# Optimization experiments

Measured on AMD Instinct MI355X. Metric: run time of the kernel, lower is better.

## Reference

```python
import jax, jax.numpy as jnp
import numpy as np

N = 50000      # nodes (single node type 'tx')
E = 400000     # edges per edge type ('fwd' and 'rev')
F_IN = 128     # input feature dim
F = 128        # cfg.gnn.dim_inner
H = 8          # attention heads
D = F // H     # per-head dim
L = 2          # cfg.gnn.layers_mp
C = 2          # dim_out (fraud logits)


def setup_inputs() -> dict:
    key = jax.random.key(0)
    k = jax.random.split(key, 12)
    f32 = jnp.float32
    g = lambda kk, sh, fan: jax.random.normal(kk, sh, f32) / np.float32(np.sqrt(fan))
    return dict(
        x=jax.random.normal(k[0], (N, F_IN), f32),
        edge_index_fwd=jax.random.randint(k[1], (2, E), 0, N),
        edge_index_rev=jax.random.randint(k[2], (2, E), 0, N),
        in_w=g(k[3], (F_IN, F), F_IN),
        in_b=jnp.zeros((F,), f32),
        kqv_w=g(k[4], (L, F, 3 * F), F),
        kqv_b=jnp.zeros((L, 3 * F), f32),
        krel_w=g(k[5], (L, 2, H, D, D), D),
        vrel_w=g(k[6], (L, 2, H, D, D), D),
        p_rel=jnp.ones((L, 2, H), f32),
        out_w=g(k[7], (L, F, F), F),
        out_b=jnp.zeros((L, F), f32),
        skip=jnp.ones((L,), f32),
        head_w=g(k[8], (F, C), F),
        head_b=jnp.zeros((C,), f32),
    )


def reference(x, edge_index_fwd, edge_index_rev, in_w, in_b, kqv_w, kqv_b,
              krel_w, vrel_w, p_rel, out_w, out_b, skip, head_w, head_b):
    n = x.shape[0]
    ef, er = edge_index_fwd, edge_index_rev
    Ef, Er = ef.shape[1], er.shape[1]
    dst = jnp.concatenate([ef[1], er[1]])                 # [E_tot]
    scale = 1.0 / jnp.sqrt(jnp.asarray(D, x.dtype))

    h = x @ in_w + in_b                                   # in_proj['tx'], [N,F]
    for l in range(L):
        kqv = h @ kqv_w[l] + kqv_b[l]                     # [N,3F]
        k, q, v = jnp.split(kqv, 3, axis=1)
        k = k.reshape(n, H, D)
        q = q.reshape(n, H, D)
        v = v.reshape(n, H, D)
        # per-edge-type relation transforms (head-wise DxD, no bias)
        k_rel = jnp.einsum('nhd,ehdf->enhf', k, krel_w[l])  # [2,N,H,D]
        v_rel = jnp.einsum('nhd,ehdf->enhf', v, vrel_w[l])
        # gather src features per edge type, concatenate edge types
        k_j = jnp.concatenate([k_rel[0][ef[0]], k_rel[1][er[0]]], axis=0)  # [E_tot,H,D]
        v_j = jnp.concatenate([v_rel[0][ef[0]], v_rel[1][er[0]]], axis=0)
        p_e = jnp.concatenate([jnp.broadcast_to(p_rel[l, 0], (Ef, H)),
                               jnp.broadcast_to(p_rel[l, 1], (Er, H))], axis=0)
        q_i = q[dst]                                       # [E_tot,H,D]
        alpha = jnp.einsum('ehd,ehd->eh', q_i, k_j) * p_e * scale
        # segment softmax over all incoming edges of each dst node
        m = jax.ops.segment_max(alpha, dst, num_segments=n)
        ex = jnp.exp(alpha - m[dst])
        denom = jax.ops.segment_sum(ex, dst, num_segments=n)
        w = ex / (denom[dst] + 1e-16)                      # [E_tot,H]
        agg = jax.ops.segment_sum(w[:, :, None] * v_j, dst,
                                  num_segments=n).reshape(n, F)
        a = jax.nn.gelu(agg, approximate=False) @ out_w[l] + out_b[l]
        g = jax.nn.sigmoid(skip[l])
        h = jax.nn.relu(g * a + (1.0 - g) * h)             # skip + act(dropout=0)
    return h @ head_w + head_b                             # logits [N,C]
```

## Files before the change

### kernel.cpp

```cpp
#include <hip/hip_runtime.h>
#include <math.h>

typedef short short8 __attribute__((ext_vector_type(8)));
typedef float f32x4 __attribute__((ext_vector_type(4)));

__device__ __forceinline__ unsigned short f2bf(float f){
    unsigned u = __float_as_uint(f);
    unsigned r = u + 0x7fffu + ((u >> 16) & 1u);
    return (unsigned short)(r >> 16);
}
__device__ __forceinline__ float bf2f(unsigned short s){
    return __uint_as_float((unsigned)s << 16);
}

__global__ void k_count(const int* __restrict__ ef, const int* __restrict__ er,
                        int* __restrict__ deg, int Ef, int Er)
{
    int Etot = Ef + Er;
    for (int e = blockIdx.x*blockDim.x + threadIdx.x; e < Etot; e += gridDim.x*blockDim.x) {
        int dst = (e < Ef) ? ef[Ef + e] : er[Er + (e - Ef)];
        atomicAdd(&deg[dst], 1);
    }
}

__global__ void k_chunk_sums(const int* __restrict__ deg, int* __restrict__ csum, int n)
{
    __shared__ int s[256];
    int t = threadIdx.x, i = blockIdx.x*256 + t;
    s[t] = (i < n) ? deg[i] : 0;
    __syncthreads();
    for (int off = 128; off > 0; off >>= 1) {
        if (t < off) s[t] += s[t + off];
        __syncthreads();
    }
    if (t == 0) csum[blockIdx.x] = s[0];
}

__global__ void k_scan_chunks(int* __restrict__ csum, int nch)
{
    __shared__ int s[1024];
    int t = threadIdx.x;
    int v = (t < nch) ? csum[t] : 0;
    s[t] = v; __syncthreads();
    for (int off = 1; off < 1024; off <<= 1) {
        int u = (t >= off) ? s[t - off] : 0;
        __syncthreads();
        s[t] += u;
        __syncthreads();
    }
    if (t < nch) csum[t] = s[t] - v;
}

__global__ void k_rowstart(const int* __restrict__ deg, const int* __restrict__ csum,
                           int* __restrict__ row_start, int* __restrict__ cursor, int n)
{
    __shared__ int s[256];
    int t = threadIdx.x, i = blockIdx.x*256 + t;
    int d = (i < n) ? deg[i] : 0;
    s[t] = d; __syncthreads();
    for (int off = 1; off < 256; off <<= 1) {
        int u = (t >= off) ? s[t - off] : 0;
        __syncthreads();
        s[t] += u;
        __syncthreads();
    }
    if (i <= n) {
        int rs = csum[blockIdx.x] + s[t] - d;
        row_start[i] = rs;
        cursor[i] = rs;
    }
}

__global__ void k_fill(const int* __restrict__ ef, const int* __restrict__ er,
                       int* __restrict__ cursor, unsigned* __restrict__ srcs,
                       int Ef, int Er, int n_nodes)
{
    int Etot = Ef + Er;
    if (blockIdx.x == 0 && threadIdx.x < 8) srcs[Etot + threadIdx.x] = 0;
    for (int e = blockIdx.x*blockDim.x + threadIdx.x; e < Etot; e += gridDim.x*blockDim.x) {
        int src, dst, tt;
        if (e < Ef) { src = ef[e]; dst = ef[Ef + e]; tt = 0; }
        else { int e2 = e - Ef; src = er[e2]; dst = er[Er + e2]; tt = 1; }
        int pos = atomicAdd(&cursor[dst], 1);
        srcs[pos] = (unsigned)(tt*n_nodes + src)*32u;
    }
}

__global__ void k_setup(const float* __restrict__ kqv_w, const float* __restrict__ kqv_b,
                        const float* __restrict__ krel_w, const float* __restrict__ vrel_w,
                        const float* __restrict__ p_rel, const float* __restrict__ out_w,
                        const float* __restrict__ out_b, const float* __restrict__ in_w,
                        const float* __restrict__ x, const float* __restrict__ head_b,
                        unsigned short* __restrict__ WcT, float* __restrict__ biasc,
                        unsigned short* __restrict__ WoT, float* __restrict__ biaso,
                        unsigned short* __restrict__ WiT, unsigned short* __restrict__ x16,
                        int* __restrict__ deg, float* __restrict__ logits, int n_nodes)
{
    const int N0 = 2*129*640;
    const int N1 = N0 + 2*129*128;
    const int N2 = N1 + 128*128;
    const long long N3 = (long long)N2 + (long long)n_nodes*32;
    const long long N4 = N3 + n_nodes;
    const long long N5 = N4 + 2*n_nodes;

    for (long long idx = (long long)blockIdx.x*blockDim.x + threadIdx.x; idx < N5;
         idx += (long long)gridDim.x*blockDim.x) {
        if (idx < N0) {
            int i = (int)idx;
            int l = i / (129*640);
            int rem = i % (129*640);
            int r = rem / 640, c = rem % 640;
            float val;
            if (c < 128) {
                val = (r < 128) ? kqv_w[((size_t)l*128 + r)*384 + 128 + c]
                                : kqv_b[l*384 + 128 + c];
            } else {
                int c2 = c - 128;
                int tt = c2 >> 8;
                int cc = c2 & 255;
                int f = cc >> 1;
                int part = cc & 1;
                int hh = f >> 4, fd = f & 15;
                const float* rw = (part == 0 ? krel_w : vrel_w)
                                  + (((size_t)(l*2 + tt)*8 + hh)*16)*16 + fd;
                int base_col = (part == 0 ? 0 : 256) + hh*16;
                float s = 0.f;
                #pragma unroll
                for (int d = 0; d < 16; ++d) {
                    float a = (r < 128) ? kqv_w[((size_t)l*128 + r)*384 + base_col + d]
                                        : kqv_b[l*384 + base_col + d];
                    s += a * rw[d*16];
                }
                if (part == 0) s *= p_rel[(l*2 + tt)*8 + hh] * 0.25f * 1.4426950408889634f;
                val = s;
            }
            if (r < 128) WcT[((size_t)l*640 + c)*128 + r] = f2bf(val);
            else         biasc[l*640 + c] = val;
        } else if (idx < N1) {
            int i = (int)(idx - N0);
            int l = i / (129*128);
            int rem = i % (129*128);
            int r = rem / 128, c = rem % 128;
            if (r < 128) WoT[((size_t)l*128 + c)*128 + r] = f2bf(out_w[((size_t)l*128 + r)*128 + c]);
            else         biaso[l*128 + c] = out_b[l*128 + c];
        } else if (idx < N2) {
            int i = (int)(idx - N1);
            int r = i >> 7, c = i & 127;
            WiT[(size_t)c*128 + r] = f2bf(in_w[(size_t)r*128 + c]);
        } else if (idx < N3) {
            long long i = idx - N2;
            float4 v = *(const float4*)&x[i*4];
            uint2 w;
            w.x = (unsigned)f2bf(v.x) | ((unsigned)f2bf(v.y) << 16);
            w.y = (unsigned)f2bf(v.z) | ((unsigned)f2bf(v.w) << 16);
            *(uint2*)&x16[i*4] = w;
        } else if (idx < N4) {
            deg[idx - N3] = 0;
        } else {
            long long i = idx - N4;
            logits[i] = head_b[i & 1];
        }
    }
}

__global__ __launch_bounds__(256) void k_mfma(
    const unsigned short* __restrict__ A16, const unsigned short* __restrict__ WT,
    const float* __restrict__ biasc, unsigned short* __restrict__ q16,
    unsigned short* __restrict__ h16, unsigned* __restrict__ kv,
    const float* __restrict__ skip, const float* __restrict__ hw,
    float* __restrict__ logits, int l,
    int n_nodes, int R, int C, int mode)
{
    __shared__ uint4 As[64*16];
    __shared__ uint4 Ws[64*16];
    int b = blockIdx.x;
    int xcd = b & 7, jj = b >> 3;
    int r_t = (jj / C)*8 + xcd;
    int c_t = jj % C;
    if (r_t >= R) return;
    int n0 = r_t*64, c0 = c_t*64;
    int t = threadIdx.x;

    #pragma unroll
    for (int it = 0; it < 4; ++it) {
        int gi = t + it*256;
        int m = gi >> 4, g = gi & 15;
        uint4 a = *(const uint4*)&A16[((size_t)(n0 + m)*16 + g)*8];
        As[m*16 + (g ^ (m & 15))] = a;
    }
    #pragma unroll
    for (int it = 0; it < 4; ++it) {
        int gi = t + it*256;
        int cw = gi >> 4, g = gi & 15;
        uint4 wv = *(const uint4*)&WT[((size_t)(c0 + cw)*16 + g)*8];
        Ws[cw*16 + (g ^ (cw & 15))] = wv;
    }
    __syncthreads();

    int lane = t & 63, w = t >> 6;
    int lm = lane & 15, quad = lane >> 4;
    f32x4 acc[4];
    #pragma unroll
    for (int i = 0; i < 4; ++i) { acc[i][0]=0.f; acc[i][1]=0.f; acc[i][2]=0.f; acc[i][3]=0.f; }

    #pragma unroll
    for (int chunk = 0; chunk < 4; ++chunk) {
        int gq = chunk*4 + quad;
        short8 bfrag = *(const short8*)&Ws[(w*16 + lm)*16 + (gq ^ lm)];
        #pragma unroll
        for (int i = 0; i < 4; ++i) {
            short8 afrag = *(const short8*)&As[(i*16 + lm)*16 + (gq ^ lm)];
            acc[i] = __builtin_amdgcn_mfma_f32_16x16x32_bf16(afrag, bfrag, acc[i], 0, 0, 0);
        }
    }

    int c = c0 + w*16 + lm;
    float bc = biasc[c];
    bool even = (lane & 1) == 0;
    if (mode == 3) {
        float g = 1.f/(1.f + expf(-skip[l]));
        float hw0 = hw[c*2], hw1 = hw[c*2 + 1];
        #pragma unroll
        for (int i = 0; i < 4; ++i) {
            #pragma unroll
            for (int rr = 0; rr < 4; ++rr) {
                int m = n0 + i*16 + quad*4 + rr;
                float nv = 0.f;
                if (m < n_nodes) {
                    float hv = bf2f(h16[(size_t)m*128 + c]);
                    nv = fmaxf(g*(acc[i][rr] + bc) + (1.f - g)*hv, 0.f);
                }
                float p0 = nv*hw0, p1 = nv*hw1;
                p0 += __shfl_xor(p0, 1); p1 += __shfl_xor(p1, 1);
                p0 += __shfl_xor(p0, 2); p1 += __shfl_xor(p1, 2);
                p0 += __shfl_xor(p0, 4); p1 += __shfl_xor(p1, 4);
                p0 += __shfl_xor(p0, 8); p1 += __shfl_xor(p1, 8);
                if (lm == 0 && m < n_nodes) {
                    atomicAdd(&logits[m*2],     p0);
                    atomicAdd(&logits[m*2 + 1], p1);
                }
            }
        }
    } else if (mode == 2) {
        float g = 1.f/(1.f + expf(-skip[l]));
        unsigned* dst = (unsigned*)h16;
        #pragma unroll
        for (int i = 0; i < 4; ++i) {
            #pragma unroll
            for (int rr = 0; rr < 4; ++rr) {
                int m = n0 + i*16 + quad*4 + rr;
                float hv = (m < n_nodes) ? bf2f(h16[(size_t)m*128 + c]) : 0.f;
                float nv = fmaxf(g*(acc[i][rr] + bc) + (1.f - g)*hv, 0.f);
                float other = __shfl_xor(nv, 1);
                if (even && m < n_nodes)
                    dst[(size_t)m*64 + (c >> 1)] =
                        (unsigned)f2bf(nv) | ((unsigned)f2bf(other) << 16);
            }
        }
    } else if (mode == 0) {
        unsigned* dst = (unsigned*)h16;
        #pragma unroll
        for (int i = 0; i < 4; ++i) {
            #pragma unroll
            for (int rr = 0; rr < 4; ++rr) {
                int m = n0 + i*16 + quad*4 + rr;
                float nv = acc[i][rr] + bc;
                float other = __shfl_xor(nv, 1);
                if (even && m < n_nodes)
                    dst[(size_t)m*64 + (c >> 1)] =
                        (unsigned)f2bf(nv) | ((unsigned)f2bf(other) << 16);
            }
        }
    } else if (c0 < 128) {
        unsigned* dst = (unsigned*)q16;
        #pragma unroll
        for (int i = 0; i < 4; ++i) {
            #pragma unroll
            for (int rr = 0; rr < 4; ++rr) {
                float val = acc[i][rr] + bc;
                float other = __shfl_xor(val, 1);
                int m = n0 + i*16 + quad*4 + rr;
                if (even && m < n_nodes)
                    dst[(size_t)m*64 + (c >> 1)] =
                        (unsigned)f2bf(val) | ((unsigned)f2bf(other) << 16);
            }
        }
    } else {
        int c2 = c - 128;
        int tt = c2 >> 8;
        int f = (c2 & 255) >> 1;
        unsigned* dst = kv + (size_t)tt*n_nodes*128;
        #pragma unroll
        for (int i = 0; i < 4; ++i) {
            #pragma unroll
            for (int rr = 0; rr < 4; ++rr) {
                float val = acc[i][rr] + bc;
                float other = __shfl_xor(val, 1);
                int m = n0 + i*16 + quad*4 + rr;
                if (even && m < n_nodes) {
                    unsigned wd = ((unsigned)f2bf(val) << 16) | (unsigned)f2bf(other);
                    dst[(size_t)m*128 + f] = wd;
                }
            }
        }
    }
}

__global__ __launch_bounds__(256) void k_attn(
    const unsigned* __restrict__ srcs, const int* __restrict__ row_start,
    const uint4* __restrict__ kv, const unsigned short* __restrict__ q16,
    unsigned short* __restrict__ qa16, int n_nodes)
{
    int lane = threadIdx.x & 31;
    int n = blockIdx.x*8 + (threadIdx.x >> 5);
    if (n >= n_nodes) return;
    uint2 qp = *(const uint2*)&q16[(size_t)n*128 + lane*4];
    float4 q4;
    q4.x = __uint_as_float(qp.x << 16);
    q4.y = __uint_as_float(qp.x & 0xffff0000u);
    q4.z = __uint_as_float(qp.y << 16);
    q4.w = __uint_as_float(qp.y & 0xffff0000u);
    int s = row_start[n], e = row_start[n + 1];

    const uint4* kvl = kv + lane;

    float lsum = 0.f;
    float4 a = make_float4(0.f, 0.f, 0.f, 0.f);

    unsigned sv0 = srcs[s],     sv1 = srcs[s + 1];
    unsigned sv2 = srcs[s + 2], sv3 = srcs[s + 3];
    uint4 w0 = kvl[sv0], w1 = kvl[sv1], w2 = kvl[sv2], w3 = kvl[sv3];

    int pos = s;

#define ATT_PAIR(wA, wB)                                                       \
    {                                                                          \
        float d0 = __uint_as_float(wA.x & 0xffff0000u)*q4.x                    \
                 + __uint_as_float(wA.y & 0xffff0000u)*q4.y                    \
                 + __uint_as_float(wA.z & 0xffff0000u)*q4.z                    \
                 + __uint_as_float(wA.w & 0xffff0000u)*q4.w;                   \
        float d1 = __uint_as_float(wB.x & 0xffff0000u)*q4.x                    \
                 + __uint_as_float(wB.y & 0xffff0000u)*q4.y                    \
                 + __uint_as_float(wB.z & 0xffff0000u)*q4.z                    \
                 + __uint_as_float(wB.w & 0xffff0000u)*q4.w;                   \
        d0 += __shfl_xor(d0, 1); d1 += __shfl_xor(d1, 1);                      \
        d0 += __shfl_xor(d0, 2); d1 += __shfl_xor(d1, 2);                      \
        float wt0 = exp2f(d0), wt1 = exp2f(d1);                                \
        lsum += wt0 + wt1;                                                     \
        a.x += wt0*__uint_as_float(wA.x << 16);                                \
        a.y += wt0*__uint_as_float(wA.y << 16);                                \
        a.z += wt0*__uint_as_float(wA.z << 16);                                \
        a.w += wt0*__uint_as_float(wA.w << 16);                                \
        a.x += wt1*__uint_as_float(wB.x << 16);                                \
        a.y += wt1*__uint_as_float(wB.y << 16);                                \
        a.z += wt1*__uint_as_float(wB.z << 16);                                \
        a.w += wt1*__uint_as_float(wB.w << 16);                                \
    }
// ... 40 lines not shown
    uint2 pk;
    pk.x = (unsigned)f2bf(g0) | ((unsigned)f2bf(g1) << 16);
    pk.y = (unsigned)f2bf(g2) | ((unsigned)f2bf(g3) << 16);
    *(uint2*)&qa16[(size_t)n*128 + lane*4] = pk;
}

extern "C" void kernel_launch(void* const* d_in, const int* in_sizes, int n_in,
                              void* d_out, int out_size, void* d_ws, size_t ws_size,
                              hipStream_t stream)
{
    const float* x      = (const float*)d_in[0];
    const int*   ef     = (const int*)d_in[1];
    const int*   er     = (const int*)d_in[2];
    const float* in_w   = (const float*)d_in[3];
    const float* in_b   = (const float*)d_in[4];
    const float* kqv_w  = (const float*)d_in[5];
    const float* kqv_b  = (const float*)d_in[6];
    const float* krel_w = (const float*)d_in[7];
    const float* vrel_w = (const float*)d_in[8];
    const float* p_rel  = (const float*)d_in[9];
    const float* out_w  = (const float*)d_in[10];
    const float* out_b  = (const float*)d_in[11];
    const float* skip   = (const float*)d_in[12];
    const float* head_w = (const float*)d_in[13];
    const float* head_b = (const float*)d_in[14];
    float* out = (float*)d_out;

    int n_nodes = in_sizes[0] / 128;
    int Ef = in_sizes[1] / 2, Er = in_sizes[2] / 2;
    int Etot = Ef + Er;
    int nch = (n_nodes + 255)/256;
    int ntile = (n_nodes + 63)/64;
    int npad = ntile*64;

    float* p = (float*)d_ws;
    unsigned* kv = (unsigned*)p; p += (size_t)2*n_nodes*128;
    unsigned short* h16  = (unsigned short*)p; p += (size_t)npad*128/2;
    unsigned short* q16  = (unsigned short*)p; p += (size_t)npad*128/2;
    unsigned short* qa16 = (unsigned short*)p; p += (size_t)npad*128/2;
    unsigned short* x16  = (unsigned short*)p; p += (size_t)npad*128/2;
    unsigned short* WiT = (unsigned short*)p; p += (size_t)(128*128)/2;
    unsigned short* WcT = (unsigned short*)p; p += (size_t)(2*640*128)/2;
    float* biasc = p; p += 2*640;
    unsigned short* WoT = (unsigned short*)p; p += (size_t)(2*128*128)/2;
    float* biaso = p; p += 2*128;
    int* deg       = (int*)p;      p += n_nodes;
    int* csum      = (int*)p;      p += 1024;
    int* row_start = (int*)p;      p += n_nodes + 1;
    int* cursor    = (int*)p;      p += n_nodes + 1;
    unsigned* srcs = (unsigned*)p; p += Etot + 8;

    int Rg = (ntile + 7)/8;

    k_setup<<<7500, 256, 0, stream>>>(kqv_w, kqv_b, krel_w, vrel_w, p_rel, out_w, out_b,
                                      in_w, x, head_b, WcT, biasc, WoT, biaso, WiT, x16,
                                      deg, out, n_nodes);
    k_count<<<1024, 256, 0, stream>>>(ef, er, deg, Ef, Er);
    k_chunk_sums<<<nch, 256, 0, stream>>>(deg, csum, n_nodes);
    k_scan_chunks<<<1, 1024, 0, stream>>>(csum, nch);
    k_rowstart<<<(n_nodes + 256)/256, 256, 0, stream>>>(deg, csum, row_start, cursor, n_nodes);
    k_fill<<<1024, 256, 0, stream>>>(ef, er, cursor, srcs, Ef, Er, n_nodes);

    k_mfma<<<Rg*8*2, 256, 0, stream>>>(x16, WiT, in_b, nullptr, h16, kv, skip,
                                       head_w, out, 0, n_nodes, ntile, 2, 0);
    for (int l = 0; l < 2; ++l) {
        k_mfma<<<Rg*8*10, 256, 0, stream>>>(h16, WcT + (size_t)l*640*128,
                                            biasc + l*640, q16, nullptr, kv, skip,
                                            head_w, out, l, n_nodes, ntile, 10, 1);
        k_attn<<<(n_nodes + 7)/8, 256, 0, stream>>>(srcs, row_start,
                                                    (const uint4*)kv, q16, qa16, n_nodes);
        int omode = (l == 1) ? 3 : 2;
        k_mfma<<<Rg*8*2, 256, 0, stream>>>(qa16, WoT + (size_t)l*128*128,
                                           biaso + l*128, nullptr, h16, kv, skip,
                                           head_w, out, l, n_nodes, ntile, 2, omode);
    }
}
```

Baseline: 432.3 us.

## Fuse CSR preprocessing into cooperative kernel and reuse A tiles across column tiles

The setup, degree count, chunk sums, chunk scan, row-start and fill kernels are merged into one cooperative kernel that uses grid-wide syncs between phases. The separate kernels remain as a fallback if the cooperative launch fails. The MFMA GEMM kernel now loops over several 64-wide column tiles per block (CF), so each A tile loaded into LDS is reused and fewer blocks are launched. This removes launch overhead and redundant A-tile loads, at the cost of grid-sync latency and fewer, longer-running GEMM blocks.

```diff
diff --git a/kernel.cpp b/kernel.cpp
--- a/kernel.cpp
+++ b/kernel.cpp
@@ -1,5 +1,8 @@
 #include <hip/hip_runtime.h>
+#include <hip/hip_cooperative_groups.h>
 #include <math.h>
+
+namespace cg = cooperative_groups;
 
 typedef short short8 __attribute__((ext_vector_type(8)));
 typedef float f32x4 __attribute__((ext_vector_type(4)));
@@ -13,74 +16,161 @@
     return __uint_as_float((unsigned)s << 16);
 }
 
-__global__ void k_count(const int* __restrict__ ef, const int* __restrict__ er,
-                        int* __restrict__ deg, int Ef, int Er)
-{
+__device__ __forceinline__ void do_setup_item(long long idx,
+        const float* __restrict__ kqv_w, const float* __restrict__ kqv_b,
+        const float* __restrict__ krel_w, const float* __restrict__ vrel_w,
+        const float* __restrict__ p_rel, const float* __restrict__ out_w,
+        const float* __restrict__ out_b, const float* __restrict__ in_w,
+        const float* __restrict__ x, const float* __restrict__ head_b,
+        unsigned short* __restrict__ WcT, float* __restrict__ biasc,
+        unsigned short* __restrict__ WoT, float* __restrict__ biaso,
+        unsigned short* __restrict__ WiT, unsigned short* __restrict__ x16,
+        int* __restrict__ deg, float* __restrict__ logits, int n_nodes)
+{
+    const int N0 = 2*129*640;
+    const int N1 = N0 + 2*129*128;
+    const int N2 = N1 + 128*128;
+    const long long N3 = (long long)N2 + (long long)n_nodes*32;
+    const long long N4 = N3 + n_nodes;
+
+    if (idx < N0) {
+        int i = (int)idx;
+        int l = i / (129*640);
+        int rem = i % (129*640);
+        int r = rem / 640, c = rem % 640;
+        float val;
+        if (c < 128) {
+            val = (r < 128) ? kqv_w[((size_t)l*128 + r)*384 + 128 + c]
+                            : kqv_b[l*384 + 128 + c];
+        } else {
+            int c2 = c - 128;
+            int tt = c2 >> 8;
+            int cc = c2 & 255;
+            int f = cc >> 1;
+            int part = cc & 1;
+            int hh = f >> 4, fd = f & 15;
+            const float* rw = (part == 0 ? krel_w : vrel_w)
+                              + (((size_t)(l*2 + tt)*8 + hh)*16)*16 + fd;
+            int base_col = (part == 0 ? 0 : 256) + hh*16;
+            float s = 0.f;
+            #pragma unroll
+            for (int d = 0; d < 16; ++d) {
+                float a = (r < 128) ? kqv_w[((size_t)l*128 + r)*384 + base_col + d]
+                                    : kqv_b[l*384 + base_col + d];
+                s += a * rw[d*16];
+            }
+            if (part == 0) s *= p_rel[(l*2 + tt)*8 + hh] * 0.25f * 1.4426950408889634f;
+            val = s;
+        }
+        if (r < 128) WcT[((size_t)l*640 + c)*128 + r] = f2bf(val);
+        else         biasc[l*640 + c] = val;
+    } else if (idx < N1) {
+        int i = (int)(idx - N0);
+        int l = i / (129*128);
+        int rem = i % (129*128);
+        int r = rem / 128, c = rem % 128;
+        if (r < 128) WoT[((size_t)l*128 + c)*128 + r] = f2bf(out_w[((size_t)l*128 + r)*128 + c]);
+        else         biaso[l*128 + c] = out_b[l*128 + c];
+    } else if (idx < N2) {
+        int i = (int)(idx - N1);
+        int r = i >> 7, c = i & 127;
+        WiT[(size_t)c*128 + r] = f2bf(in_w[(size_t)r*128 + c]);
+    } else if (idx < N3) {
+        long long i = idx - N2;
+        float4 v = *(const float4*)&x[i*4];
+        uint2 w;
+        w.x = (unsigned)f2bf(v.x) | ((unsigned)f2bf(v.y) << 16);
+        w.y = (unsigned)f2bf(v.z) | ((unsigned)f2bf(v.w) << 16);
+        *(uint2*)&x16[i*4] = w;
+    } else if (idx < N4) {
+        deg[idx - N3] = 0;
+    } else {
+        long long i = idx - N4;
+        logits[i] = head_b[i & 1];
+    }
+}
+
+__global__ __launch_bounds__(256, 4) void k_prep(
+        const float* kqv_w, const float* kqv_b, const float* krel_w, const float* vrel_w,
+        const float* p_rel, const float* out_w, const float* out_b, const float* in_w,
+        const float* x, const float* head_b,
+        unsigned short* WcT, float* biasc, unsigned short* WoT, float* biaso,
+        unsigned short* WiT, unsigned short* x16,
+        int* deg, float* logits,
+        const int* ef, const int* er,
+        int* csum, int* row_start, int* cursor, unsigned* srcs,
+        int n_nodes, int Ef, int Er, int nch)
+{
+    cg::grid_group grid = cg::this_grid();
+    __shared__ int s[256];
+    int t = threadIdx.x;
+    long long gtid = (long long)blockIdx.x*blockDim.x + t;
+    long long gstride = (long long)gridDim.x*blockDim.x;
     int Etot = Ef + Er;
-    for (int e = blockIdx.x*blockDim.x + threadIdx.x; e < Etot; e += gridDim.x*blockDim.x) {
+
+    const long long N5 = (long long)(2*129*640 + 2*129*128 + 128*128)
+                       + (long long)n_nodes*32 + n_nodes + 2*n_nodes;
+    if (blockIdx.x == 0 && t < 8) srcs[Etot + t] = 0;
+    for (long long idx = gtid; idx < N5; idx += gstride)
+        do_setup_item(idx, kqv_w, kqv_b, krel_w, vrel_w, p_rel, out_w, out_b, in_w,
+                      x, head_b, WcT, biasc, WoT, biaso, WiT, x16, deg, logits, n_nodes);
+    grid.sync();
+
+    for (long long e = gtid; e < Etot; e += gstride) {
         int dst = (e < Ef) ? ef[Ef + e] : er[Er + (e - Ef)];
         atomicAdd(&deg[dst], 1);
     }
-}
-
-__global__ void k_chunk_sums(const int* __restrict__ deg, int* __restrict__ csum, int n)
-{
-    __shared__ int s[256];
-    int t = threadIdx.x, i = blockIdx.x*256 + t;
-    s[t] = (i < n) ? deg[i] : 0;
-    __syncthreads();
-    for (int off = 128; off > 0; off >>= 1) {
-        if (t < off) s[t] += s[t + off];
-        __syncthreads();
-    }
-    if (t == 0) csum[blockIdx.x] = s[0];
-}
-
-__global__ void k_scan_chunks(int* __restrict__ csum, int nch)
-{
-    __shared__ int s[1024];
-    int t = threadIdx.x;
-    int v = (t < nch) ? csum[t] : 0;
-    s[t] = v; __syncthreads();
-    for (int off = 1; off < 1024; off <<= 1) {
-        int u = (t >= off) ? s[t - off] : 0;
-        __syncthreads();
-        s[t] += u;
-        __syncthreads();
-    }
-    if (t < nch) csum[t] = s[t] - v;
-}
-
-__global__ void k_rowstart(const int* __restrict__ deg, const int* __restrict__ csum,
-                           int* __restrict__ row_start, int* __restrict__ cursor, int n)
-{
-    __shared__ int s[256];
-    int t = threadIdx.x, i = blockIdx.x*256 + t;
-    int d = (i < n) ? deg[i] : 0;
-    s[t] = d; __syncthreads();
-    for (int off = 1; off < 256; off <<= 1) {
-        int u = (t >= off) ? s[t - off] : 0;
-        __syncthreads();
-        s[t] += u;
-        __syncthreads();
-    }
-    if (i <= n) {
-        int rs = csum[blockIdx.x] + s[t] - d;
-        row_start[i] = rs;
-        cursor[i] = rs;
-    }
-}
-
-__global__ void k_fill(const int* __restrict__ ef, const int* __restrict__ er,
-                       int* __restrict__ cursor, unsigned* __restrict__ srcs,
-                       int Ef, int Er, int n_nodes)
-{
-    int Etot = Ef + Er;
-    if (blockIdx.x == 0 && threadIdx.x < 8) srcs[Etot + threadIdx.x] = 0;
-    for (int e = blockIdx.x*blockDim.x + threadIdx.x; e < Etot; e += gridDim.x*blockDim.x) {
+    grid.sync();
+
+    for (int c = blockIdx.x; c < nch; c += gridDim.x) {
+        int i = c*256 + t;
+        s[t] = (i < n_nodes) ? deg[i] : 0;
+        __syncthreads();
+        for (int off = 128; off > 0; off >>= 1) {
+            if (t < off) s[t] += s[t + off];
+            __syncthreads();
+        }
+        if (t == 0) csum[c] = s[0];
+        __syncthreads();
+    }
+    grid.sync();
+
+    if (blockIdx.x == 0) {
+        int v = (t < nch) ? csum[t] : 0;
+        s[t] = v; __syncthreads();
+        for (int off = 1; off < 256; off <<= 1) {
+            int u = (t >= off) ? s[t - off] : 0;
+            __syncthreads();
+            s[t] += u;
+            __syncthreads();
+        }
+        if (t < nch) csum[t] = s[t] - v;
+    }
+    grid.sync();
+
+    for (int c = blockIdx.x; c < nch; c += gridDim.x) {
+        int i = c*256 + t;
+        int d = (i < n_nodes) ? deg[i] : 0;
+        s[t] = d; __syncthreads();
+        for (int off = 1; off < 256; off <<= 1) {
+            int u = (t >= off) ? s[t - off] : 0;
+            __syncthreads();
+            s[t] += u;
+            __syncthreads();
+        }
+        if (i <= n_nodes) {
+            int rs = csum[c] + s[t] - d;
+            row_start[i] = rs;
+            cursor[i] = rs;
+        }
+        __syncthreads();
+    }
+    grid.sync();
+
+    for (long long e = gtid; e < Etot; e += gstride) {
         int src, dst, tt;
         if (e < Ef) { src = ef[e]; dst = ef[Ef + e]; tt = 0; }
-        else { int e2 = e - Ef; src = er[e2]; dst = er[Er + e2]; tt = 1; }
+        else { long long e2 = e - Ef; src = er[e2]; dst = er[Er + e2]; tt = 1; }
         int pos = atomicAdd(&cursor[dst], 1);
         srcs[pos] = (unsigned)(tt*n_nodes + src)*32u;
     }
@@ -96,70 +186,84 @@
                         unsigned short* __restrict__ WiT, unsigned short* __restrict__ x16,
                         int* __restrict__ deg, float* __restrict__ logits, int n_nodes)
 {
-    const int N0 = 2*129*640;
-    const int N1 = N0 + 2*129*128;
-    const int N2 = N1 + 128*128;
-    const long long N3 = (long long)N2 + (long long)n_nodes*32;
-    const long long N4 = N3 + n_nodes;
-    const long long N5 = N4 + 2*n_nodes;
-
+    const long long N5 = (long long)(2*129*640 + 2*129*128 + 128*128)
+                       + (long long)n_nodes*32 + n_nodes + 2*n_nodes;
     for (long long idx = (long long)blockIdx.x*blockDim.x + threadIdx.x; idx < N5;
-         idx += (long long)gridDim.x*blockDim.x) {
-        if (idx < N0) {
-            int i = (int)idx;
-            int l = i / (129*640);
-            int rem = i % (129*640);
-            int r = rem / 640, c = rem % 640;
-            float val;
-            if (c < 128) {
-                val = (r < 128) ? kqv_w[((size_t)l*128 + r)*384 + 128 + c]
-                                : kqv_b[l*384 + 128 + c];
-            } else {
-                int c2 = c - 128;
-                int tt = c2 >> 8;
-                int cc = c2 & 255;
-                int f = cc >> 1;
-                int part = cc & 1;
-                int hh = f >> 4, fd = f & 15;
-                const float* rw = (part == 0 ? krel_w : vrel_w)
-                                  + (((size_t)(l*2 + tt)*8 + hh)*16)*16 + fd;
-                int base_col = (part == 0 ? 0 : 256) + hh*16;
-                float s = 0.f;
-                #pragma unroll
-                for (int d = 0; d < 16; ++d) {
-                    float a = (r < 128) ? kqv_w[((size_t)l*128 + r)*384 + base_col + d]
-                                        : kqv_b[l*384 + base_col + d];
-                    s += a * rw[d*16];
-                }
-                if (part == 0) s *= p_rel[(l*2 + tt)*8 + hh] * 0.25f * 1.4426950408889634f;
-                val = s;
-            }
-            if (r < 128) WcT[((size_t)l*640 + c)*128 + r] = f2bf(val);
-            else         biasc[l*640 + c] = val;
-        } else if (idx < N1) {
-            int i = (int)(idx - N0);
-            int l = i / (129*128);
-            int rem = i % (129*128);
-            int r = rem / 128, c = rem % 128;
-            if (r < 128) WoT[((size_t)l*128 + c)*128 + r] = f2bf(out_w[((size_t)l*128 + r)*128 + c]);
-            else         biaso[l*128 + c] = out_b[l*128 + c];
-        } else if (idx < N2) {
-            int i = (int)(idx - N1);
-            int r = i >> 7, c = i & 127;
-            WiT[(size_t)c*128 + r] = f2bf(in_w[(size_t)r*128 + c]);
-        } else if (idx < N3) {
-            long long i = idx - N2;
-            float4 v = *(const float4*)&x[i*4];
-            uint2 w;
-            w.x = (unsigned)f2bf(v.x) | ((unsigned)f2bf(v.y) << 16);
-            w.y = (unsigned)f2bf(v.z) | ((unsigned)f2bf(v.w) << 16);
-            *(uint2*)&x16[i*4] = w;
-        } else if (idx < N4) {
-            deg[idx - N3] = 0;
-        } else {
-            long long i = idx - N4;
-            logits[i] = head_b[i & 1];
-        }
+         idx += (long long)gridDim.x*blockDim.x)
+        do_setup_item(idx, kqv_w, kqv_b, krel_w, vrel_w, p_rel, out_w, out_b, in_w,
+                      x, head_b, WcT, biasc, WoT, biaso, WiT, x16, deg, logits, n_nodes);
+}
+
+__global__ void k_count(const int* __restrict__ ef, const int* __restrict__ er,
+                        int* __restrict__ deg, int Ef, int Er)
+{
+    int Etot = Ef + Er;
+    for (int e = blockIdx.x*blockDim.x + threadIdx.x; e < Etot; e += gridDim.x*blockDim.x) {
+        int dst = (e < Ef) ? ef[Ef + e] : er[Er + (e - Ef)];
+        atomicAdd(&deg[dst], 1);
+    }
+}
+
+__global__ void k_chunk_sums(const int* __restrict__ deg, int* __restrict__ csum, int n)
+{
+    __shared__ int s[256];
+    int t = threadIdx.x, i = blockIdx.x*256 + t;
+    s[t] = (i < n) ? deg[i] : 0;
+    __syncthreads();
+    for (int off = 128; off > 0; off >>= 1) {
+        if (t < off) s[t] += s[t + off];
+        __syncthreads();
+    }
+    if (t == 0) csum[blockIdx.x] = s[0];
+}
+
+__global__ void k_scan_chunks(int* __restrict__ csum, int nch)
+{
+    __shared__ int s[1024];
+    int t = threadIdx.x;
+    int v = (t < nch) ? csum[t] : 0;
+    s[t] = v; __syncthreads();
+    for (int off = 1; off < 1024; off <<= 1) {
+        int u = (t >= off) ? s[t - off] : 0;
+        __syncthreads();
+        s[t] += u;
+        __syncthreads();
+    }
+    if (t < nch) csum[t] = s[t] - v;
+}
+
+__global__ void k_rowstart(const int* __restrict__ deg, const int* __restrict__ csum,
+                           int* __restrict__ row_start, int* __restrict__ cursor, int n)
+{
+    __shared__ int s[256];
+    int t = threadIdx.x, i = blockIdx.x*256 + t;
+    int d = (i < n) ? deg[i] : 0;
+    s[t] = d; __syncthreads();
+    for (int off = 1; off < 256; off <<= 1) {
+        int u = (t >= off) ? s[t - off] : 0;
+        __syncthreads();
+        s[t] += u;
+        __syncthreads();
+    }
+    if (i <= n) {
+        int rs = csum[blockIdx.x] + s[t] - d;
+        row_start[i] = rs;
+        cursor[i] = rs;
+    }
+}
+
+__global__ void k_fill(const int* __restrict__ ef, const int* __restrict__ er,
+                       int* __restrict__ cursor, unsigned* __restrict__ srcs,
+                       int Ef, int Er, int n_nodes)
+{
+    int Etot = Ef + Er;
+    if (blockIdx.x == 0 && threadIdx.x < 8) srcs[Etot + threadIdx.x] = 0;
+    for (int e = blockIdx.x*blockDim.x + threadIdx.x; e < Etot; e += gridDim.x*blockDim.x) {
+        int src, dst, tt;
+        if (e < Ef) { src = ef[e]; dst = ef[Ef + e]; tt = 0; }
+        else { int e2 = e - Ef; src = er[e2]; dst = er[Er + e2]; tt = 1; }
+        int pos = atomicAdd(&cursor[dst], 1);
+        srcs[pos] = (unsigned)(tt*n_nodes + src)*32u;
     }
 }
 
@@ -169,16 +273,17 @@
     unsigned short* __restrict__ h16, unsigned* __restrict__ kv,
     const float* __restrict__ skip, const float* __restrict__ hw,
     float* __restrict__ logits, int l,
-    int n_nodes, int R, int C, int mode)
+    int n_nodes, int R, int C, int CF, int mode)
 {
     __shared__ uint4 As[64*16];
     __shared__ uint4 Ws[64*16];
+    int G = C / CF;
     int b = blockIdx.x;
     int xcd = b & 7, jj = b >> 3;
-    int r_t = (jj / C)*8 + xcd;
-    int c_t = jj % C;
+    int r_t = (jj / G)*8 + xcd;
+    int g_t = jj % G;
     if (r_t >= R) return;
-    int n0 = r_t*64, c0 = c_t*64;
+    int n0 = r_t*64;
     int t = threadIdx.x;
 
     #pragma unroll
@@ -188,121 +293,128 @@
         uint4 a = *(const uint4*)&A16[((size_t)(n0 + m)*16 + g)*8];
         As[m*16 + (g ^ (m & 15))] = a;
     }
-    #pragma unroll
-    for (int it = 0; it < 4; ++it) {
-        int gi = t + it*256;
-        int cw = gi >> 4, g = gi & 15;
-        uint4 wv = *(const uint4*)&WT[((size_t)(c0 + cw)*16 + g)*8];
-        Ws[cw*16 + (g ^ (cw & 15))] = wv;
-    }
-    __syncthreads();
 
     int lane = t & 63, w = t >> 6;
     int lm = lane & 15, quad = lane >> 4;
-    f32x4 acc[4];
-    #pragma unroll
-    for (int i = 0; i < 4; ++i) { acc[i][0]=0.f; acc[i][1]=0.f; acc[i][2]=0.f; acc[i][3]=0.f; }
-
-    #pragma unroll
-    for (int chunk = 0; chunk < 4; ++chunk) {
-        int gq = chunk*4 + quad;
-        short8 bfrag = *(const short8*)&Ws[(w*16 + lm)*16 + (gq ^ lm)];
+    bool even = (lane & 1) == 0;
+
+    for (int cf = 0; cf < CF; ++cf) {
+        int c0 = (g_t*CF + cf)*64;
+
         #pragma unroll
-        for (int i = 0; i < 4; ++i) {
-            short8 afrag = *(const short8*)&As[(i*16 + lm)*16 + (gq ^ lm)];
-            acc[i] = __builtin_amdgcn_mfma_f32_16x16x32_bf16(afrag, bfrag, acc[i], 0, 0, 0);
-        }
-    }
-
-    int c = c0 + w*16 + lm;
-    float bc = biasc[c];
-    bool even = (lane & 1) == 0;
-    if (mode == 3) {
-        float g = 1.f/(1.f + expf(-skip[l]));
-        float hw0 = hw[c*2], hw1 = hw[c*2 + 1];
+        for (int it = 0; it < 4; ++it) {
+            int gi = t + it*256;
+            int cw = gi >> 4, g = gi & 15;
+            uint4 wv = *(const uint4*)&WT[((size_t)(c0 + cw)*16 + g)*8];
+            Ws[cw*16 + (g ^ (cw & 15))] = wv;
+        }
+        __syncthreads();
+
+        f32x4 acc[4];
         #pragma unroll
-        for (int i = 0; i < 4; ++i) {
+        for (int i = 0; i < 4; ++i) { acc[i][0]=0.f; acc[i][1]=0.f; acc[i][2]=0.f; acc[i][3]=0.f; }
+
+        #pragma unroll
+        for (int chunk = 0; chunk < 4; ++chunk) {
+            int gq = chunk*4 + quad;
+            short8 bfrag = *(const short8*)&Ws[(w*16 + lm)*16 + (gq ^ lm)];
             #pragma unroll
-            for (int rr = 0; rr < 4; ++rr) {
-                int m = n0 + i*16 + quad*4 + rr;
-                float nv = 0.f;
-                if (m < n_nodes) {
-                    float hv = bf2f(h16[(size_t)m*128 + c]);
-                    nv = fmaxf(g*(acc[i][rr] + bc) + (1.f - g)*hv, 0.f);
-                }
-                float p0 = nv*hw0, p1 = nv*hw1;
-                p0 += __shfl_xor(p0, 1); p1 += __shfl_xor(p1, 1);
-                p0 += __shfl_xor(p0, 2); p1 += __shfl_xor(p1, 2);
-                p0 += __shfl_xor(p0, 4); p1 += __shfl_xor(p1, 4);
-                p0 += __shfl_xor(p0, 8); p1 += __shfl_xor(p1, 8);
-                if (lm == 0 && m < n_nodes) {
-                    atomicAdd(&logits[m*2],     p0);
-                    atomicAdd(&logits[m*2 + 1], p1);
+            for (int i = 0; i < 4; ++i) {
+                short8 afrag = *(const short8*)&As[(i*16 + lm)*16 + (gq ^ lm)];
+                acc[i] = __builtin_amdgcn_mfma_f32_16x16x32_bf16(afrag, bfrag, acc[i], 0, 0, 0);
+            }
+        }
+
+        int c = c0 + w*16 + lm;
+        float bc = biasc[c];
+        if (mode == 3) {
+            float g = 1.f/(1.f + expf(-skip[l]));
+            float hw0 = hw[c*2], hw1 = hw[c*2 + 1];
+            #pragma unroll
+            for (int i = 0; i < 4; ++i) {
+                #pragma unroll
+                for (int rr = 0; rr < 4; ++rr) {
+                    int m = n0 + i*16 + quad*4 + rr;
+                    float nv = 0.f;
+                    if (m < n_nodes) {
+                        float hv = bf2f(h16[(size_t)m*128 + c]);
+                        nv = fmaxf(g*(acc[i][rr] + bc) + (1.f - g)*hv, 0.f);
+                    }
+                    float p0 = nv*hw0, p1 = nv*hw1;
+                    p0 += __shfl_xor(p0, 1); p1 += __shfl_xor(p1, 1);
+                    p0 += __shfl_xor(p0, 2); p1 += __shfl_xor(p1, 2);
+                    p0 += __shfl_xor(p0, 4); p1 += __shfl_xor(p1, 4);
+                    p0 += __shfl_xor(p0, 8); p1 += __shfl_xor(p1, 8);
+                    if (lm == 0 && m < n_nodes) {
+                        atomicAdd(&logits[m*2],     p0);
+                        atomicAdd(&logits[m*2 + 1], p1);
+                    }
                 }
             }
-        }
-    } else if (mode == 2) {
-        float g = 1.f/(1.f + expf(-skip[l]));
-        unsigned* dst = (unsigned*)h16;
-        #pragma unroll
-        for (int i = 0; i < 4; ++i) {
+        } else if (mode == 2) {
+            float g = 1.f/(1.f + expf(-skip[l]));
+            unsigned* dst = (unsigned*)h16;
             #pragma unroll
-            for (int rr = 0; rr < 4; ++rr) {
-                int m = n0 + i*16 + quad*4 + rr;
-                float hv = (m < n_nodes) ? bf2f(h16[(size_t)m*128 + c]) : 0.f;
-                float nv = fmaxf(g*(acc[i][rr] + bc) + (1.f - g)*hv, 0.f);
-                float other = __shfl_xor(nv, 1);
-                if (even && m < n_nodes)
-                    dst[(size_t)m*64 + (c >> 1)] =
-                        (unsigned)f2bf(nv) | ((unsigned)f2bf(other) << 16);
-            }
-        }
-    } else if (mode == 0) {
-        unsigned* dst = (unsigned*)h16;
-        #pragma unroll
-        for (int i = 0; i < 4; ++i) {
-            #pragma unroll
-            for (int rr = 0; rr < 4; ++rr) {
-                int m = n0 + i*16 + quad*4 + rr;
-                float nv = acc[i][rr] + bc;
-                float other = __shfl_xor(nv, 1);
-                if (even && m < n_nodes)
-                    dst[(size_t)m*64 + (c >> 1)] =
-                        (unsigned)f2bf(nv) | ((unsigned)f2bf(other) << 16);
-            }
-        }
-    } else if (c0 < 128) {
-        unsigned* dst = (unsigned*)q16;
-        #pragma unroll
-        for (int i = 0; i < 4; ++i) {
-            #pragma unroll
-            for (int rr = 0; rr < 4; ++rr) {
-                float val = acc[i][rr] + bc;
-                float other = __shfl_xor(val, 1);
-                int m = n0 + i*16 + quad*4 + rr;
-                if (even && m < n_nodes)
-                    dst[(size_t)m*64 + (c >> 1)] =
-                        (unsigned)f2bf(val) | ((unsigned)f2bf(other) << 16);
-            }
-        }
-    } else {
-        int c2 = c - 128;
-        int tt = c2 >> 8;
-        int f = (c2 & 255) >> 1;
-        unsigned* dst = kv + (size_t)tt*n_nodes*128;
-        #pragma unroll
-        for (int i = 0; i < 4; ++i) {
-            #pragma unroll
-            for (int rr = 0; rr < 4; ++rr) {
-                float val = acc[i][rr] + bc;
-                float other = __shfl_xor(val, 1);
-                int m = n0 + i*16 + quad*4 + rr;
-                if (even && m < n_nodes) {
-                    unsigned wd = ((unsigned)f2bf(val) << 16) | (unsigned)f2bf(other);
-                    dst[(size_t)m*128 + f] = wd;
+            for (int i = 0; i < 4; ++i) {
+                #pragma unroll
+                for (int rr = 0; rr < 4; ++rr) {
+                    int m = n0 + i*16 + quad*4 + rr;
+                    float hv = (m < n_nodes) ? bf2f(h16[(size_t)m*128 + c]) : 0.f;
+                    float nv = fmaxf(g*(acc[i][rr] + bc) + (1.f - g)*hv, 0.f);
+                    float other = __shfl_xor(nv, 1);
+                    if (even && m < n_nodes)
+                        dst[(size_t)m*64 + (c >> 1)] =
+                            (unsigned)f2bf(nv) | ((unsigned)f2bf(other) << 16);
                 }
             }
-        }
+        } else if (mode == 0) {
+            unsigned* dst = (unsigned*)h16;
+            #pragma unroll
+            for (int i = 0; i < 4; ++i) {
+                #pragma unroll
+                for (int rr = 0; rr < 4; ++rr) {
+                    int m = n0 + i*16 + quad*4 + rr;
+                    float nv = acc[i][rr] + bc;
+                    float other = __shfl_xor(nv, 1);
+                    if (even && m < n_nodes)
+                        dst[(size_t)m*64 + (c >> 1)] =
+                            (unsigned)f2bf(nv) | ((unsigned)f2bf(other) << 16);
+                }
+            }
+        } else if (c0 < 128) {
+            unsigned* dst = (unsigned*)q16;
+            #pragma unroll
+            for (int i = 0; i < 4; ++i) {
+                #pragma unroll
+                for (int rr = 0; rr < 4; ++rr) {
+                    float val = acc[i][rr] + bc;
+                    float other = __shfl_xor(val, 1);
+                    int m = n0 + i*16 + quad*4 + rr;
+                    if (even && m < n_nodes)
+                        dst[(size_t)m*64 + (c >> 1)] =
+                            (unsigned)f2bf(val) | ((unsigned)f2bf(other) << 16);
+                }
+            }
+        } else {
+            int c2 = c - 128;
+            int tt = c2 >> 8;
+            int f = (c2 & 255) >> 1;
+            unsigned* dst = kv + (size_t)tt*n_nodes*128;
+            #pragma unroll
+            for (int i = 0; i < 4; ++i) {
+                #pragma unroll
+                for (int rr = 0; rr < 4; ++rr) {
+                    float val = acc[i][rr] + bc;
+                    float other = __shfl_xor(val, 1);
+                    int m = n0 + i*16 + quad*4 + rr;
+                    if (even && m < n_nodes) {
+                        unsigned wd = ((unsigned)f2bf(val) << 16) | (unsigned)f2bf(other);
+                        dst[(size_t)m*128 + f] = wd;
+                    }
+                }
+            }
+        }
+        __syncthreads();
     }
 }
 
@@ -449,26 +561,43 @@
 
     int Rg = (ntile + 7)/8;
 
-    k_setup<<<7500, 256, 0, stream>>>(kqv_w, kqv_b, krel_w, vrel_w, p_rel, out_w, out_b,
-                                      in_w, x, head_b, WcT, biasc, WoT, biaso, WiT, x16,
-                                      deg, out, n_nodes);
-    k_count<<<1024, 256, 0, stream>>>(ef, er, deg, Ef, Er);
-    k_chunk_sums<<<nch, 256, 0, stream>>>(deg, csum, n_nodes);
-    k_scan_chunks<<<1, 1024, 0, stream>>>(csum, nch);
-    k_rowstart<<<(n_nodes + 256)/256, 256, 0, stream>>>(deg, csum, row_start, cursor, n_nodes);
-    k_fill<<<1024, 256, 0, stream>>>(ef, er, cursor, srcs, Ef, Er, n_nodes);
-
-    k_mfma<<<Rg*8*2, 256, 0, stream>>>(x16, WiT, in_b, nullptr, h16, kv, skip,
-                                       head_w, out, 0, n_nodes, ntile, 2, 0);
+    {
+        void* args[] = {
+            (void*)&kqv_w, (void*)&kqv_b, (void*)&krel_w, (void*)&vrel_w,
+            (void*)&p_rel, (void*)&out_w, (void*)&out_b, (void*)&in_w,
+            (void*)&x, (void*)&head_b,
+            (void*)&WcT, (void*)&biasc, (void*)&WoT, (void*)&biaso,
+            (void*)&WiT, (void*)&x16,
+            (void*)&deg, (void*)&out,
+            (void*)&ef, (void*)&er,
+            (void*)&csum, (void*)&row_start, (void*)&cursor, (void*)&srcs,
+            (void*)&n_nodes, (void*)&Ef, (void*)&Er, (void*)&nch
+        };
+        hipError_t ce = hipLaunchCooperativeKernel((const void*)k_prep, dim3(512), dim3(256),
+                                                   args, 0u, stream);
+        if (ce != hipSuccess) {
+            k_setup<<<7500, 256, 0, stream>>>(kqv_w, kqv_b, krel_w, vrel_w, p_rel, out_w, out_b,
+                                              in_w, x, head_b, WcT, biasc, WoT, biaso, WiT, x16,
+                                              deg, out, n_nodes);
+            k_count<<<1024, 256, 0, stream>>>(ef, er, deg, Ef, Er);
+            k_chunk_sums<<<nch, 256, 0, stream>>>(deg, csum, n_nodes);
+            k_scan_chunks<<<1, 1024, 0, stream>>>(csum, nch);
+            k_rowstart<<<(n_nodes + 256)/256, 256, 0, stream>>>(deg, csum, row_start, cursor, n_nodes);
+            k_fill<<<1024, 256, 0, stream>>>(ef, er, cursor, srcs, Ef, Er, n_nodes);
+        }
+    }
+
+    k_mfma<<<Rg*8, 256, 0, stream>>>(x16, WiT, in_b, nullptr, h16, kv, skip,
+                                     head_w, out, 0, n_nodes, ntile, 2, 2, 0);
     for (int l = 0; l < 2; ++l) {
-        k_mfma<<<Rg*8*10, 256, 0, stream>>>(h16, WcT + (size_t)l*640*128,
-                                            biasc + l*640, q16, nullptr, kv, skip,
-                                            head_w, out, l, n_nodes, ntile, 10, 1);
+        k_mfma<<<Rg*8*2, 256, 0, stream>>>(h16, WcT + (size_t)l*640*128,
+                                           biasc + l*640, q16, nullptr, kv, skip,
+                                           head_w, out, l, n_nodes, ntile, 10, 5, 1);
         k_attn<<<(n_nodes + 7)/8, 256, 0, stream>>>(srcs, row_start,
                                                     (const uint4*)kv, q16, qa16, n_nodes);
         int omode = (l == 1) ? 3 : 2;
-        k_mfma<<<Rg*8*2, 256, 0, stream>>>(qa16, WoT + (size_t)l*128*128,
-                                           biaso + l*128, nullptr, h16, kv, skip,
-                                           head_w, out, l, n_nodes, ntile, 2, omode);
-    }
-}
+        k_mfma<<<Rg*8, 256, 0, stream>>>(qa16, WoT + (size_t)l*128*128,
+                                         biaso + l*128, nullptr, h16, kv, skip,
+                                         head_w, out, l, n_nodes, ntile, 2, 2, omode);
+    }
+}
```

Result: slower. 792.1 us (+83.2%).

## Reuse A tile across column tiles with double-buffered direct-to-LDS weight loads

Applied to the files above, without the earlier changes.

Each GEMM block now loops over several 64-wide output column tiles (CF) and reuses one A tile staged in LDS, instead of one block per column tile. Weight tiles are double-buffered and prefetched with global_load_lds, so the next tile streams straight into LDS while the current one is computed. The swizzle moves to the global-address side. This cuts redundant A-tile reloads and launches far fewer blocks, at the cost of less parallelism per kernel and an extra barrier per column tile.

```diff
diff --git a/kernel.cpp b/kernel.cpp
--- a/kernel.cpp
+++ b/kernel.cpp
@@ -11,6 +11,12 @@
 }
 __device__ __forceinline__ float bf2f(unsigned short s){
     return __uint_as_float((unsigned)s << 16);
+}
+
+__device__ __forceinline__ void gload16(const void* g, void* l){
+    __builtin_amdgcn_global_load_lds(
+        (const __attribute__((address_space(1))) unsigned*)g,
+        (__attribute__((address_space(3))) unsigned*)l, 16, 0, 0);
 }
 
 __global__ void k_count(const int* __restrict__ ef, const int* __restrict__ er,
@@ -169,140 +175,162 @@
     unsigned short* __restrict__ h16, unsigned* __restrict__ kv,
     const float* __restrict__ skip, const float* __restrict__ hw,
     float* __restrict__ logits, int l,
-    int n_nodes, int R, int C, int mode)
+    int n_nodes, int R, int C, int CF, int mode)
 {
     __shared__ uint4 As[64*16];
-    __shared__ uint4 Ws[64*16];
+    __shared__ uint4 Ws[2][64*16];
+    int G = C / CF;
     int b = blockIdx.x;
     int xcd = b & 7, jj = b >> 3;
-    int r_t = (jj / C)*8 + xcd;
-    int c_t = jj % C;
+    int r_t = (jj / G)*8 + xcd;
+    int g_t = jj % G;
     if (r_t >= R) return;
-    int n0 = r_t*64, c0 = c_t*64;
+    int n0 = r_t*64;
     int t = threadIdx.x;
 
     #pragma unroll
     for (int it = 0; it < 4; ++it) {
         int gi = t + it*256;
-        int m = gi >> 4, g = gi & 15;
-        uint4 a = *(const uint4*)&A16[((size_t)(n0 + m)*16 + g)*8];
-        As[m*16 + (g ^ (m & 15))] = a;
-    }
-    #pragma unroll
-    for (int it = 0; it < 4; ++it) {
-        int gi = t + it*256;
-        int cw = gi >> 4, g = gi & 15;
-        uint4 wv = *(const uint4*)&WT[((size_t)(c0 + cw)*16 + g)*8];
-        Ws[cw*16 + (g ^ (cw & 15))] = wv;
+        int m = gi >> 4, gs = gi & 15;
+        int g = gs ^ (m & 15);
+        gload16(&A16[((size_t)(n0 + m)*16 + g)*8], &As[gi]);
+    }
+    {
+        int c0 = (g_t*CF)*64;
+        #pragma unroll
+        for (int it = 0; it < 4; ++it) {
+            int gi = t + it*256;
+            int cw = gi >> 4, gs = gi & 15;
+            int g = gs ^ (cw & 15);
+            gload16(&WT[((size_t)(c0 + cw)*16 + g)*8], &Ws[0][gi]);
+        }
     }
     __syncthreads();
 
     int lane = t & 63, w = t >> 6;
     int lm = lane & 15, quad = lane >> 4;
-    f32x4 acc[4];
-    #pragma unroll
-    for (int i = 0; i < 4; ++i) { acc[i][0]=0.f; acc[i][1]=0.f; acc[i][2]=0.f; acc[i][3]=0.f; }
-
-    #pragma unroll
-    for (int chunk = 0; chunk < 4; ++chunk) {
-        int gq = chunk*4 + quad;
-        short8 bfrag = *(const short8*)&Ws[(w*16 + lm)*16 + (gq ^ lm)];
+    bool even = (lane & 1) == 0;
+
+    for (int cf = 0; cf < CF; ++cf) {
+        int buf = cf & 1;
+        if (cf + 1 < CF) {
+            int c0n = (g_t*CF + cf + 1)*64;
+            #pragma unroll
+            for (int it = 0; it < 4; ++it) {
+                int gi = t + it*256;
+                int cw = gi >> 4, gs = gi & 15;
+                int g = gs ^ (cw & 15);
+                gload16(&WT[((size_t)(c0n + cw)*16 + g)*8], &Ws[buf ^ 1][gi]);
+            }
+        }
+
+        int c0 = (g_t*CF + cf)*64;
+
+        f32x4 acc[4];
         #pragma unroll
-        for (int i = 0; i < 4; ++i) {
-            short8 afrag = *(const short8*)&As[(i*16 + lm)*16 + (gq ^ lm)];
-            acc[i] = __builtin_amdgcn_mfma_f32_16x16x32_bf16(afrag, bfrag, acc[i], 0, 0, 0);
+        for (int i = 0; i < 4; ++i) { acc[i][0]=0.f; acc[i][1]=0.f; acc[i][2]=0.f; acc[i][3]=0.f; }
+
+        #pragma unroll
+        for (int chunk = 0; chunk < 4; ++chunk) {
+            int gq = chunk*4 + quad;
+            short8 bfrag = *(const short8*)&Ws[buf][(w*16 + lm)*16 + (gq ^ lm)];
+            #pragma unroll
+            for (int i = 0; i < 4; ++i) {
+                short8 afrag = *(const short8*)&As[(i*16 + lm)*16 + (gq ^ lm)];
+                acc[i] = __builtin_amdgcn_mfma_f32_16x16x32_bf16(afrag, bfrag, acc[i], 0, 0, 0);
+            }
         }
-    }
-
-    int c = c0 + w*16 + lm;
-    float bc = biasc[c];
-    bool even = (lane & 1) == 0;
-    if (mode == 3) {
-        float g = 1.f/(1.f + expf(-skip[l]));
-        float hw0 = hw[c*2], hw1 = hw[c*2 + 1];
-        #pragma unroll
-        for (int i = 0; i < 4; ++i) {
-            #pragma unroll
-            for (int rr = 0; rr < 4; ++rr) {
-                int m = n0 + i*16 + quad*4 + rr;
-                float nv = 0.f;
-                if (m < n_nodes) {
-                    float hv = bf2f(h16[(size_t)m*128 + c]);
-                    nv = fmaxf(g*(acc[i][rr] + bc) + (1.f - g)*hv, 0.f);
+
+        int c = c0 + w*16 + lm;
+        float bc = biasc[c];
+        if (mode == 3) {
+            float g = 1.f/(1.f + expf(-skip[l]));
+            float hw0 = hw[c*2], hw1 = hw[c*2 + 1];
+            #pragma unroll
+            for (int i = 0; i < 4; ++i) {
+                #pragma unroll
+                for (int rr = 0; rr < 4; ++rr) {
+                    int m = n0 + i*16 + quad*4 + rr;
+                    float nv = 0.f;
+                    if (m < n_nodes) {
+                        float hv = bf2f(h16[(size_t)m*128 + c]);
+                        nv = fmaxf(g*(acc[i][rr] + bc) + (1.f - g)*hv, 0.f);
+                    }
+                    float p0 = nv*hw0, p1 = nv*hw1;
+                    p0 += __shfl_xor(p0, 1); p1 += __shfl_xor(p1, 1);
+                    p0 += __shfl_xor(p0, 2); p1 += __shfl_xor(p1, 2);
+                    p0 += __shfl_xor(p0, 4); p1 += __shfl_xor(p1, 4);
+                    p0 += __shfl_xor(p0, 8); p1 += __shfl_xor(p1, 8);
+                    if (lm == 0 && m < n_nodes) {
+                        atomicAdd(&logits[m*2],     p0);
+                        atomicAdd(&logits[m*2 + 1], p1);
+                    }
                 }
-                float p0 = nv*hw0, p1 = nv*hw1;
-                p0 += __shfl_xor(p0, 1); p1 += __shfl_xor(p1, 1);
-                p0 += __shfl_xor(p0, 2); p1 += __shfl_xor(p1, 2);
-                p0 += __shfl_xor(p0, 4); p1 += __shfl_xor(p1, 4);
-                p0 += __shfl_xor(p0, 8); p1 += __shfl_xor(p1, 8);
-                if (lm == 0 && m < n_nodes) {
-                    atomicAdd(&logits[m*2],     p0);
-                    atomicAdd(&logits[m*2 + 1], p1);
+            }
+        } else if (mode == 2) {
+            float g = 1.f/(1.f + expf(-skip[l]));
+            unsigned* dst = (unsigned*)h16;
+            #pragma unroll
+            for (int i = 0; i < 4; ++i) {
+                #pragma unroll
+                for (int rr = 0; rr < 4; ++rr) {
+                    int m = n0 + i*16 + quad*4 + rr;
+                    float hv = (m < n_nodes) ? bf2f(h16[(size_t)m*128 + c]) : 0.f;
+                    float nv = fmaxf(g*(acc[i][rr] + bc) + (1.f - g)*hv, 0.f);
+                    float other = __shfl_xor(nv, 1);
+                    if (even && m < n_nodes)
+                        dst[(size_t)m*64 + (c >> 1)] =
+                            (unsigned)f2bf(nv) | ((unsigned)f2bf(other) << 16);
                 }
             }
+        } else if (mode == 0) {
+            unsigned* dst = (unsigned*)h16;
+            #pragma unroll
+            for (int i = 0; i < 4; ++i) {
+                #pragma unroll
+                for (int rr = 0; rr < 4; ++rr) {
+                    int m = n0 + i*16 + quad*4 + rr;
+                    float nv = acc[i][rr] + bc;
+                    float other = __shfl_xor(nv, 1);
+                    if (even && m < n_nodes)
+                        dst[(size_t)m*64 + (c >> 1)] =
+                            (unsigned)f2bf(nv) | ((unsigned)f2bf(other) << 16);
+                }
+            }
+        } else if (c0 < 128) {
+            unsigned* dst = (unsigned*)q16;
+            #pragma unroll
+            for (int i = 0; i < 4; ++i) {
+                #pragma unroll
+                for (int rr = 0; rr < 4; ++rr) {
+                    float val = acc[i][rr] + bc;
+                    float other = __shfl_xor(val, 1);
+                    int m = n0 + i*16 + quad*4 + rr;
+                    if (even && m < n_nodes)
+                        dst[(size_t)m*64 + (c >> 1)] =
+                            (unsigned)f2bf(val) | ((unsigned)f2bf(other) << 16);
+                }
+            }
+        } else {
+            int c2 = c - 128;
+            int tt = c2 >> 8;
+            int f = (c2 & 255) >> 1;
+            unsigned* dst = kv + (size_t)tt*n_nodes*128;
+            #pragma unroll
+            for (int i = 0; i < 4; ++i) {
+                #pragma unroll
+                for (int rr = 0; rr < 4; ++rr) {
+                    float val = acc[i][rr] + bc;
+                    float other = __shfl_xor(val, 1);
+                    int m = n0 + i*16 + quad*4 + rr;
+                    if (even && m < n_nodes) {
+                        unsigned wd = ((unsigned)f2bf(val) << 16) | (unsigned)f2bf(other);
+                        dst[(size_t)m*128 + f] = wd;
+                    }
+                }
+            }
         }
-    } else if (mode == 2) {
-        float g = 1.f/(1.f + expf(-skip[l]));
-        unsigned* dst = (unsigned*)h16;
-        #pragma unroll
-        for (int i = 0; i < 4; ++i) {
-            #pragma unroll
-            for (int rr = 0; rr < 4; ++rr) {
-                int m = n0 + i*16 + quad*4 + rr;
-                float hv = (m < n_nodes) ? bf2f(h16[(size_t)m*128 + c]) : 0.f;
-                float nv = fmaxf(g*(acc[i][rr] + bc) + (1.f - g)*hv, 0.f);
-                float other = __shfl_xor(nv, 1);
-                if (even && m < n_nodes)
-                    dst[(size_t)m*64 + (c >> 1)] =
-                        (unsigned)f2bf(nv) | ((unsigned)f2bf(other) << 16);
-            }
-        }
-    } else if (mode == 0) {
-        unsigned* dst = (unsigned*)h16;
-        #pragma unroll
-        for (int i = 0; i < 4; ++i) {
-            #pragma unroll
-            for (int rr = 0; rr < 4; ++rr) {
-                int m = n0 + i*16 + quad*4 + rr;
-                float nv = acc[i][rr] + bc;
-                float other = __shfl_xor(nv, 1);
-                if (even && m < n_nodes)
-                    dst[(size_t)m*64 + (c >> 1)] =
-                        (unsigned)f2bf(nv) | ((unsigned)f2bf(other) << 16);
-            }
-        }
-    } else if (c0 < 128) {
-        unsigned* dst = (unsigned*)q16;
-        #pragma unroll
-        for (int i = 0; i < 4; ++i) {
-            #pragma unroll
-            for (int rr = 0; rr < 4; ++rr) {
-                float val = acc[i][rr] + bc;
-                float other = __shfl_xor(val, 1);
-                int m = n0 + i*16 + quad*4 + rr;
-                if (even && m < n_nodes)
-                    dst[(size_t)m*64 + (c >> 1)] =
-                        (unsigned)f2bf(val) | ((unsigned)f2bf(other) << 16);
-            }
-        }
-    } else {
-        int c2 = c - 128;
-        int tt = c2 >> 8;
-        int f = (c2 & 255) >> 1;
-        unsigned* dst = kv + (size_t)tt*n_nodes*128;
-        #pragma unroll
-        for (int i = 0; i < 4; ++i) {
-            #pragma unroll
-            for (int rr = 0; rr < 4; ++rr) {
-                float val = acc[i][rr] + bc;
-                float other = __shfl_xor(val, 1);
-                int m = n0 + i*16 + quad*4 + rr;
-                if (even && m < n_nodes) {
-                    unsigned wd = ((unsigned)f2bf(val) << 16) | (unsigned)f2bf(other);
-                    dst[(size_t)m*128 + f] = wd;
-                }
-            }
-        }
+        __syncthreads();
     }
 }
 
@@ -458,17 +486,17 @@
     k_rowstart<<<(n_nodes + 256)/256, 256, 0, stream>>>(deg, csum, row_start, cursor, n_nodes);
     k_fill<<<1024, 256, 0, stream>>>(ef, er, cursor, srcs, Ef, Er, n_nodes);
 
-    k_mfma<<<Rg*8*2, 256, 0, stream>>>(x16, WiT, in_b, nullptr, h16, kv, skip,
-                                       head_w, out, 0, n_nodes, ntile, 2, 0);
+    k_mfma<<<Rg*8, 256, 0, stream>>>(x16, WiT, in_b, nullptr, h16, kv, skip,
+                                     head_w, out, 0, n_nodes, ntile, 2, 2, 0);
     for (int l = 0; l < 2; ++l) {
-        k_mfma<<<Rg*8*10, 256, 0, stream>>>(h16, WcT + (size_t)l*640*128,
-                                            biasc + l*640, q16, nullptr, kv, skip,
-                                            head_w, out, l, n_nodes, ntile, 10, 1);
+        k_mfma<<<Rg*8*2, 256, 0, stream>>>(h16, WcT + (size_t)l*640*128,
+                                           biasc + l*640, q16, nullptr, kv, skip,
+                                           head_w, out, l, n_nodes, ntile, 10, 5, 1);
         k_attn<<<(n_nodes + 7)/8, 256, 0, stream>>>(srcs, row_start,
                                                     (const uint4*)kv, q16, qa16, n_nodes);
         int omode = (l == 1) ? 3 : 2;
-        k_mfma<<<Rg*8*2, 256, 0, stream>>>(qa16, WoT + (size_t)l*128*128,
-                                           biaso + l*128, nullptr, h16, kv, skip,
-                                           head_w, out, l, n_nodes, ntile, 2, omode);
-    }
-}
+        k_mfma<<<Rg*8, 256, 0, stream>>>(qa16, WoT + (size_t)l*128*128,
+                                         biaso + l*128, nullptr, h16, kv, skip,
+                                         head_w, out, l, n_nodes, ntile, 2, 2, omode);
+    }
+}
```

Result: slower. 493.2 us (+14.1%).
